# Kernel optimization log

Measured on AMD Instinct MI355X. Metric: run time of the kernel, lower is better.

Reference implementation:

```python
import jax, jax.numpy as jnp
import numpy as np
import math

D_HEAD = 64  # scaling uses sqrt(d_head), NOT sqrt of full projection dim (faithful to source)

def setup_inputs() -> dict:
    key = jax.random.key(0)
    ks = jax.random.split(key, 9)
    B, S, D = 4, 2048, 1024
    s = 0.02
    return {
        "x": jax.random.normal(ks[0], (B, S, D), dtype=jnp.float32),
        "Wq": jax.random.normal(ks[1], (D, D), dtype=jnp.float32) * s,
        "bq": jax.random.normal(ks[2], (D,), dtype=jnp.float32) * s,
        "Wk": jax.random.normal(ks[3], (D, D), dtype=jnp.float32) * s,
        "bk": jax.random.normal(ks[4], (D,), dtype=jnp.float32) * s,
        "Wv": jax.random.normal(ks[5], (D, D), dtype=jnp.float32) * s,
        "bv": jax.random.normal(ks[6], (D,), dtype=jnp.float32) * s,
        "Wo": jax.random.normal(ks[7], (D, D), dtype=jnp.float32) * s,
        "bo": jax.random.normal(ks[8], (D,), dtype=jnp.float32) * s,
    }

def reference(x, Wq, bq, Wk, bk, Wv, bv, Wo, bo):
    # Q/K/V projections: [B,S,D] @ [D,D] + b
    Q = jnp.einsum('bsd,de->bse', x, Wq) + bq
    K = jnp.einsum('bsd,de->bse', x, Wk) + bk
    V = jnp.einsum('bsd,de->bse', x, Wv) + bv
    # NOTE: source does bmm over the FULL projected dim (no head split),
    # scaled by sqrt(d_head) only.
    scores = jnp.einsum('bqd,bkd->bqk', Q, K) / math.sqrt(D_HEAD)  # [B,S,S]
    S_len = scores.shape[-1]
    causal = jnp.tril(jnp.ones((S_len, S_len), dtype=bool))
    scores = jnp.where(causal, scores, -jnp.inf)
    weights = jax.nn.softmax(scores, axis=-1)
    attn_out = jnp.einsum('bqk,bkd->bqd', weights, V)
    return jnp.einsum('bsd,de->bse', attn_out, Wo) + bo
```

## Files before the change

kernel.cpp:

```cpp
#include <hip/hip_runtime.h>
#include <stdint.h>

typedef _Float16 f16;
typedef __attribute__((ext_vector_type(8))) _Float16 f16x8;
typedef __attribute__((ext_vector_type(4))) _Float16 f16x4;
typedef __attribute__((ext_vector_type(4))) float f32x4;

typedef __attribute__((address_space(3))) uint32_t lds_u32;
typedef const __attribute__((address_space(1))) uint32_t glb_u32;

__device__ __forceinline__ void gload_lds16(const void* g, void* l) {
    __builtin_amdgcn_global_load_lds((glb_u32*)g, (lds_u32*)l, 16, 0, 0);
}


template<int ROWS>
__device__ __forceinline__
void stage2(const f16* __restrict__ G, int ldg, f16* lds,
            int grow0, int k0, int tid)
{
    const int l = tid & 63, w = tid >> 6;
    #pragma unroll
    for (int q = 0; q < ROWS / 32; ++q) {
        const int r = q * 32 + w * 8 + (l >> 3);
        const int csw = (((l & 7) ^ (r & 7)) << 3);
        gload_lds16(G + (long long)(grow0 + r) * ldg + (k0 + csw),
                    lds + q * 2048 + w * 512);
    }
}

template<int OUT_MODE, int CAUSAL, int TM, int TN>
__device__ __forceinline__
void gemm2_body(const f16* __restrict__ A, const f16* __restrict__ B,
                const float* __restrict__ bias, void* __restrict__ Cv,
                int M, int N, int K,
                long long sAb, long long sBb, long long sCb, float scale,
                int bx, int by, int bzi)
{
    constexpr int IM = TM / 32;
    constexpr int JN = TN / 32;

    int mtile, n0;
    if (CAUSAL == 1) {
        int rem = bx, mi = 0;
        while (rem > mi) { rem -= mi + 1; ++mi; }
        mtile = mi;
        n0 = rem * TN;
    } else {
        mtile = by;
        n0 = bx * TN;
    }

    const int tid  = threadIdx.x;
    const int wave = tid >> 6;
    const int lane = tid & 63;
    const long long bz = bzi;
    A += bz * sAb;
    B += bz * sBb;

    __shared__ f16 As[2][TM * 64];
    __shared__ f16 Bs[2][TN * 64];

    const int fr  = lane & 15;
    const int hk  = lane >> 4;
    const int lsw = lane & 7;
    const int wm  = (wave >> 1) * (TM / 2);
    const int wn  = (wave & 1) * (TN / 2);

    const int npass = (CAUSAL == 2) ? 2 : 1;
    for (int pass = 0; pass < npass; ++pass) {
        const int mt = (CAUSAL == 2 && pass == 1) ? (M / TM - 1 - mtile) : mtile;
        const int m0 = mt * TM;
        const int Kend = (CAUSAL == 2) ? (m0 + TM) : K;

        f32x4 acc[IM][JN] = {};

        stage2<TM>(A, K, &As[0][0], m0, 0, tid);
        stage2<TN>(B, K, &Bs[0][0], n0, 0, tid);
        asm volatile("s_waitcnt vmcnt(0)" ::: "memory");
        __builtin_amdgcn_s_barrier();

        int cur = 0;
        for (int k0 = 0; k0 < Kend; k0 += 64) {
            if (k0 + 64 < Kend) {
                stage2<TM>(A, K, &As[cur ^ 1][0], m0, k0 + 64, tid);
                stage2<TN>(B, K, &Bs[cur ^ 1][0], n0, k0 + 64, tid);
            }

            f16x8 af[IM][2], bf[JN][2];
            #pragma unroll
            for (int i = 0; i < IM; ++i)
                #pragma unroll
                for (int kk = 0; kk < 2; ++kk)
                    af[i][kk] = *(const f16x8*)((const char*)&As[cur][0] +
                        ((wm + i * 16 + fr) << 7) +
                        ((((kk << 2) | hk) ^ lsw) << 4));
            #pragma unroll
            for (int j = 0; j < JN; ++j)
                #pragma unroll
                for (int kk = 0; kk < 2; ++kk)
                    bf[j][kk] = *(const f16x8*)((const char*)&Bs[cur][0] +
                        ((wn + j * 16 + fr) << 7) +
                        ((((kk << 2) | hk) ^ lsw) << 4));

            asm volatile("s_waitcnt lgkmcnt(0)" ::: "memory");
            __builtin_amdgcn_s_setprio(1);
            #pragma unroll
            for (int i = 0; i < IM; ++i)
                #pragma unroll
                for (int j = 0; j < JN; ++j)
                    #pragma unroll
                    for (int kk = 0; kk < 2; ++kk)
                        acc[i][j] = __builtin_amdgcn_mfma_f32_16x16x32_f16(
                            af[i][kk], bf[j][kk], acc[i][j], 0, 0, 0);
            __builtin_amdgcn_s_setprio(0);

            asm volatile("s_waitcnt vmcnt(0)" ::: "memory");
            __builtin_amdgcn_s_barrier();
            cur ^= 1;
        }

        const int cn = lane & 15;
        const int cm = (lane >> 4) * 4;
        #pragma unroll
        for (int j = 0; j < JN; ++j) {
            const int gn = n0 + wn + j * 16 + cn;
            #pragma unroll
            for (int i = 0; i < IM; ++i) {
                const int gm = m0 + wm + i * 16 + cm;
                if (OUT_MODE == 0) {
                    const float bv = bias ? bias[gn] : 0.f;
                    float* C = (float*)Cv + bz * sCb;
                    #pragma unroll
                    for (int r = 0; r < 4; ++r)
                        C[(long long)(gm + r) * N + gn] = acc[i][j][r] * scale + bv;
                } else {
                    const float bv = bias ? bias[(long long)bz * N + gn] : 0.f;
                    f16* C = (f16*)Cv + bz * sCb;
                    #pragma unroll
                    for (int r = 0; r < 4; ++r)
                        C[(long long)(gm + r) * N + gn] = (f16)(acc[i][j][r] * scale + bv);
                }
            }
        }
    }
}

template<int OUT_MODE, int CAUSAL, int TM, int TN>
__global__ __launch_bounds__(256, 2)
void gemm2_bt(const f16* __restrict__ A, const f16* __restrict__ B,
              const float* __restrict__ bias, void* __restrict__ Cv,
              int M, int N, int K,
              long long sAb, long long sBb, long long sCb, float scale)
{
    gemm2_body<OUT_MODE, CAUSAL, TM, TN>(A, B, bias, Cv, M, N, K,
                                         sAb, sBb, sCb, scale,
                                         blockIdx.x, blockIdx.y, blockIdx.z);
}


__device__ __forceinline__
void stage_half(const f16* __restrict__ G, int ldg, f16* lds_half,
                int grow0, int k0, int tid)
{
    const int lr  = tid >> 3;
    const int csw = ((tid & 7) * 8) ^ ((lr & 7) << 3);
    gload_lds16(G + (long long)(grow0 + lr) * ldg + (k0 + csw),
                lds_half + ((tid >> 6) << 9));
    gload_lds16(G + (long long)(grow0 + 64 + lr) * ldg + (k0 + csw),
                lds_half + 4096 + ((tid >> 6) << 9));
}

template<int MODE>
__global__ __launch_bounds__(512, 2)
void gemm256_4ph(const f16* __restrict__ A, const f16* __restrict__ B,
                 const float* __restrict__ bias, const float* __restrict__ bias2,
                 f16* __restrict__ C0, f16* __restrict__ C1,
                 int M, int N, int K,
                 long long sAb, long long sBb, long long sCb, float scale)
{
    __shared__ f16 lds[65536];

    const int nwg  = gridDim.x;
    const int orig = blockIdx.x;
    const int swz  = (orig & 7) * (nwg >> 3) + (orig >> 3);

    int m0, n0;
    long long bz = 0;
    if (MODE == 1) {
        const int nr  = M >> 8;
        const int per = nr * (nr + 1) / 2;
        bz = swz / per;
        int rem = swz - (int)bz * per, mi = 0;
        while (rem > mi) { rem -= mi + 1; ++mi; }
        m0 = mi << 8;
        n0 = rem << 8;
    } else {
        const int ntn = N >> 8;
        const int mt = swz / ntn, nt = swz - mt * ntn;
        m0 = mt << 8;
        n0 = nt << 8;
    }
    A += bz * sAb;
    B += bz * sBb;

    const int tid  = threadIdx.x;
    const int lane = tid & 63;
    const int wave = tid >> 6;
    const int wm = (wave >> 2) << 7;
    const int wn = (wave & 3) << 6;
    const int fr  = lane & 15;
    const int hk  = lane >> 4;
    const int lsw = lane & 7;
    const int nkt = K >> 6;

    f32x4 acc[8][4] = {};
    f16x8 bf[4][2];

    stage_half(A, K, lds,         m0,       0, tid);
    stage_half(A, K, lds + 8192,  m0 + 128, 0, tid);
    stage_half(B, K, lds + 32768, n0,       0, tid);
    stage_half(B, K, lds + 40960, n0 + 128, 0, tid);
    if (nkt > 1) {
        stage_half(B, K, lds + 49152, n0,       64, tid);
        stage_half(B, K, lds + 57344, n0 + 128, 64, tid);
        asm volatile("s_waitcnt vmcnt(4)" ::: "memory");
    } else {
        asm volatile("s_waitcnt vmcnt(0)" ::: "memory");
    }
    __builtin_amdgcn_s_barrier();

    for (int t = 0; t < nkt; ++t) {
        const f16* Ab = lds + (t & 1) * 16384;
        const f16* Bb = lds + 32768 + (t & 1) * 16384;
        #pragma unroll
        for (int p = 0; p < 4; ++p) {
            if (p == 0) {
                #pragma unroll
                for (int j = 0; j < 4; ++j)
                    #pragma unroll
                    for (int kk = 0; kk < 2; ++kk)
                        bf[j][kk] = *(const f16x8*)((const char*)Bb +
                            ((wn + j * 16 + fr) << 7) +
                            ((((kk << 2) | hk) ^ lsw) << 4));
            }
            f16x8 af[2][2];
            #pragma unroll
            for (int ii = 0; ii < 2; ++ii)
                #pragma unroll
                for (int kk = 0; kk < 2; ++kk)
                    af[ii][kk] = *(const f16x8*)((const char*)Ab +
                        ((wm + (2 * p + ii) * 16 + fr) << 7) +
                        ((((kk << 2) | hk) ^ lsw) << 4));

            if (p == 0 && t + 1 < nkt)
                stage_half(A, K, lds + ((t + 1) & 1) * 16384,        m0,       (t + 1) << 6, tid);
            if (p == 1 && t + 1 < nkt)
                stage_half(A, K, lds + ((t + 1) & 1) * 16384 + 8192, m0 + 128, (t + 1) << 6, tid);
            if (p == 2 && t + 2 < nkt)
                stage_half(B, K, lds + 32768 + (t & 1) * 16384,        n0,       (t + 2) << 6, tid);
            if (p == 3 && t + 2 < nkt)
                stage_half(B, K, lds + 32768 + (t & 1) * 16384 + 8192, n0 + 128, (t + 2) << 6, tid);

            if (p == 0) asm volatile("s_waitcnt lgkmcnt(8)" ::: "memory");
            __builtin_amdgcn_s_barrier();
            asm volatile("s_waitcnt lgkmcnt(0)" ::: "memory");
            __builtin_amdgcn_s_setprio(1);
            #pragma unroll
            for (int ii = 0; ii < 2; ++ii)
                #pragma unroll
                for (int j = 0; j < 4; ++j)
                    #pragma unroll
                    for (int kk = 0; kk < 2; ++kk)
                        acc[2 * p + ii][j] = __builtin_amdgcn_mfma_f32_16x16x32_f16(
                            af[ii][kk], bf[j][kk], acc[2 * p + ii][j], 0, 0, 0);
            __builtin_amdgcn_s_setprio(0);
            if (p == 3) {
                if (t + 2 < nkt) asm volatile("s_waitcnt vmcnt(4)" ::: "memory");
                else             asm volatile("s_waitcnt vmcnt(0)" ::: "memory");
            }
            __builtin_amdgcn_s_barrier();
        }
    }

    const int cn  = lane & 15;
    const int cm4 = (lane >> 4) * 4;

    if (MODE == 3 && (n0 >> 10)) {
        const int nn0 = n0 & 1023;
        const int b   = m0 >> 11, s0v = m0 & 2047;
        #pragma unroll
        for (int j = 0; j < 4; ++j) {
            const int nn_l = wn + j * 16 + cn;
            const float bb = bias2[nn0 + nn_l];
            const int X = (nn_l & 7) << 4;
            #pragma unroll
            for (int i = 0; i < 8; ++i) {
                const int s_l = wm + i * 16 + cm4;
                f16x4 pk;
                #pragma unroll
                for (int r = 0; r < 4; ++r)
                    pk[r] = (f16)(acc[i][j][r] + bb);
                *(f16x4*)((char*)lds + nn_l * 512 + ((s_l * 2) ^ X)) = pk;
            }
        }
        __syncthreads();
        #pragma unroll 4
        for (int rr = 0; rr < 32; ++rr) {
            const int nn_l = rr * 8 + wave;
            const int X = (nn_l & 7) << 4;
            const f16x4 v = *(const f16x4*)((const char*)lds + nn_l * 512 + ((lane * 8) ^ X));
            *(f16x4*)&C1[(long long)b * 2097152 + (long long)(nn0 + nn_l) * 2048 + s0v + lane * 4] = v;
        }
        return;
    }

    #pragma unroll
    for (int j = 0; j < 4; ++j) {
        const int gn = n0 + wn + j * 16 + cn;
        if (MODE == 3) {
            const int nn = gn & 1023;
            #pragma unroll
            for (int i = 0; i < 8; ++i) {
                const int gm = m0 + wm + i * 16 + cm4;
                #pragma unroll
                for (int r = 0; r < 4; ++r)
                    C0[(long long)(gm + r) * 1024 + nn] = (f16)acc[i][j][r];
            }
        } else {
            const float cbv = bias ? bias[bz * N + gn] : 0.f;
            f16* Cc = C0 + bz * sCb;
            #pragma unroll
            for (int i = 0; i < 8; ++i) {
                const int gm = m0 + wm + i * 16 + cm4;
                #pragma unroll
                for (int r = 0; r < 4; ++r)
                    Cc[(long long)(gm + r) * N + gn] = (f16)(acc[i][j][r] * scale + cbv);
            }
        }
    }
}

__global__ __launch_bounds__(256)
void prep(const float* __restrict__ x,  const float* __restrict__ Wq,
          const float* __restrict__ bq, const float* __restrict__ Wk,
          const float* __restrict__ Wv, const float* __restrict__ bv,
          const float* __restrict__ Wo,
          f16* __restrict__ xb,  f16* __restrict__ Wqf, f16* __restrict__ Wkf,
          f16* __restrict__ Wvf, f16* __restrict__ Wot,
          float* __restrict__ bvo, float* __restrict__ wvec)
{
    __shared__ f16 tile[32][33];
    __shared__ float red[4][64];
    const int t = threadIdx.x;
    int id = blockIdx.x;

    if (id < 8192) {
        const int i = (id * 256 + t) * 4;
        const float4 v = *(const float4*)&x[i];
        f16x4 o; o[0]=(f16)v.x; o[1]=(f16)v.y; o[2]=(f16)v.z; o[3]=(f16)v.w;
        *(f16x4*)&xb[i] = o;
        return;
    }
    id -= 8192;
    if (id < 3072) {
        const float* src = (id < 1024) ? Wq : (id < 2048) ? Wk : Wv;
        f16* dst = (id < 1024) ? Wqf : (id < 2048) ? Wkf : Wvf;
        const int i = ((id & 1023) * 256 + t) * 4;
        const float4 v = *(const float4*)&src[i];
        f16x4 o; o[0]=(f16)v.x; o[1]=(f16)v.y; o[2]=(f16)v.z; o[3]=(f16)v.w;
        *(f16x4*)&dst[i] = o;
        return;
    }
    id -= 3072;
    if (id < 1024) {
        const int bx = (id & 31) * 32, by = (id >> 5) * 32;
        const int tx = t & 31, ty = t >> 5;
        #pragma unroll
        for (int i = 0; i < 32; i += 8)
            tile[ty + i][tx] = (f16)Wo[(long long)(by + ty + i) * 1024 + (bx + tx)];
        __syncthreads();
        #pragma unroll
        for (int i = 0; i < 32; i += 8)
            Wot[(long long)(bx + ty + i) * 1024 + (by + tx)] = tile[tx][ty + i];
        return;
    }
    id -= 1024;
    if (id < 16) {
        const int e0 = id * 64;
        const int wave = t >> 6, lane = t & 63;
        float a0 = 0.f, a1 = 0.f, a2 = 0.f, a3 = 0.f;
        for (int i = 0; i < 256; i += 4) {
            const int k = wave * 256 + i;
            a0 += bv[k]     * Wo[(long long)k * 1024 + e0 + lane];
            a1 += bv[k + 1] * Wo[(long long)(k + 1) * 1024 + e0 + lane];
            a2 += bv[k + 2] * Wo[(long long)(k + 2) * 1024 + e0 + lane];
            a3 += bv[k + 3] * Wo[(long long)(k + 3) * 1024 + e0 + lane];
        }
        red[wave][lane] = (a0 + a1) + (a2 + a3);
        __syncthreads();
        if (wave == 0)
            bvo[e0 + lane] = red[0][lane] + red[1][lane] + red[2][lane] + red[3][lane];
        return;
    }
    id -= 16;
    {
        const int row = id * 4 + (t >> 6);
        const int lane = t & 63;
        const float* src = Wk + (long long)row * 1024;
        float a = 0.f;
        #pragma unroll
        for (int tt = 0; tt < 16; ++tt) a += src[lane + 64 * tt] * bq[lane + 64 * tt];
        #pragma unroll
        for (int o = 32; o > 0; o >>= 1) a += __shfl_down(a, o);
        if (lane == 0) wvec[row] = a * 0.125f;
    }
}

__global__ __launch_bounds__(256, 2)
void dual_weights_cvec(const f16* __restrict__ Wkf, const f16* __restrict__ Wqf,
                       const f16* __restrict__ Wot, const f16* __restrict__ Wvf,
                       f16* __restrict__ Wcat2,
                       const f16* __restrict__ xb, const float* __restrict__ wvec,
                       float* __restrict__ cbias)
{
    if (blockIdx.z == 2) {
        const int flat = blockIdx.y * 8 + blockIdx.x;
        const int wave = threadIdx.x >> 6, lane = threadIdx.x & 63;
        #pragma unroll 4
        for (int rr = 0; rr < 32; ++rr) {
            const int row = (flat * 4 + wave) * 32 + rr;
            const f16* src = xb + (long long)row * 1024;
            float a = 0.f;
            #pragma unroll
            for (int tt = 0; tt < 16; ++tt)
                a += (float)src[lane + 64 * tt] * wvec[lane + 64 * tt];
            #pragma unroll
            for (int o = 32; o > 0; o >>= 1) a += __shfl_down(a, o);
            if (lane == 0) cbias[row] = a;
        }
        return;
    }
    const f16* Ax = (blockIdx.z == 0) ? Wkf : Wot;
    const f16* Bx = (blockIdx.z == 0) ? Wqf : Wvf;
    f16* Cx = Wcat2 + (long long)blockIdx.z * 1024 * 1024;
    gemm2_body<1, 0, 128, 128>(Ax, Bx, nullptr, Cx,
                               1024, 1024, 1024, 0, 0, 0, 1.f,
                               blockIdx.x, blockIdx.y, 0);
}

__global__ __launch_bounds__(256)
void softmax_causal(const f16* __restrict__ Sc, f16* __restrict__ P, int S)
{
    const long long row = blockIdx.x;
    const int q = (int)(row % S);
    const f16* src = Sc + row * S;
    f16* dst = P + row * S;
    const int t = threadIdx.x;
    __shared__ float redm[4], reds[4];

    f16x8 vv = {};
    if (t * 8 <= q) vv = *(const f16x8*)&src[t * 8];
    float v[8];
    float mx = -3.0e38f;
    #pragma unroll
    for (int i = 0; i < 8; ++i) {
        const int k = t * 8 + i;
        v[i] = (float)vv[i];
        if (k <= q) mx = fmaxf(mx, v[i]);
    }
    #pragma unroll
    for (int o = 32; o > 0; o >>= 1) mx = fmaxf(mx, __shfl_down(mx, o));
    if ((t & 63) == 0) redm[t >> 6] = mx;
    __syncthreads();
    mx = fmaxf(fmaxf(redm[0], redm[1]), fmaxf(redm[2], redm[3]));

    float sum = 0.f;
    #pragma unroll
    for (int i = 0; i < 8; ++i) {
        const int k = t * 8 + i;
        v[i] = (k <= q) ? __expf(v[i] - mx) : 0.f;
        sum += v[i];
    }
    #pragma unroll
    for (int o = 32; o > 0; o >>= 1) sum += __shfl_down(sum, o);
    if ((t & 63) == 0) reds[t >> 6] = sum;
    __syncthreads();
    sum = reds[0] + reds[1] + reds[2] + reds[3];
    const float inv = 1.f / sum;
    const int kend = ((q >> 7) + 1) << 7;
    if (t * 8 < kend) {
        f16x8 ov;
        #pragma unroll
        for (int i = 0; i < 8; ++i) ov[i] = (f16)(v[i] * inv);
        *(f16x8*)&dst[t * 8] = ov;
    }
}

extern "C" void kernel_launch(void* const* d_in, const int* in_sizes, int n_in,
                              void* d_out, int out_size, void* d_ws, size_t ws_size,
                              hipStream_t stream)
{
    const float* x  = (const float*)d_in[0];
    const float* Wq = (const float*)d_in[1];
    const float* bq = (const float*)d_in[2];
    const float* Wk = (const float*)d_in[3];
    const float* Wv = (const float*)d_in[5];
    const float* bv = (const float*)d_in[6];
    const float* Wo = (const float*)d_in[7];
    const float* bo = (const float*)d_in[8];
    float* out = (float*)d_out;

    const int B = 4, S = 2048, D = 1024;
    const long long SD  = (long long)S * D;
    const long long SS  = (long long)S * S;
    const long long BSD = (long long)B * SD;
    const int MS = B * S;

    char* p = (char*)d_ws;
    f16*   xb    = (f16*)p;  p += BSD * 2;
    f16*   Wqf   = (f16*)p;  p += (long long)D * D * 2;
    f16*   Wkf   = (f16*)p;  p += (long long)D * D * 2;
    f16*   Wvf   = (f16*)p;  p += (long long)D * D * 2;
    f16*   Wot   = (f16*)p;  p += (long long)D * D * 2;
    f16*   Wcat2 = (f16*)p;  p += 2LL * D * D * 2;
    float* bvo   = (float*)p; p += D * 4;
    float* wvec  = (float*)p; p += D * 4;
    float* cbias = (float*)p; p += (long long)MS * 4;
    f16*   Qh    = (f16*)p;  p += BSD * 2;
    f16*   Vt    = (f16*)p;  p += BSD * 2;
    f16*   Sc    = (f16*)p;  p += (long long)B * SS * 2;
    f16*   Pb    = (f16*)p;  p += (long long)B * SS * 2;

    dim3 blk(256);

    prep<<<dim3(12560), blk, 0, stream>>>(x, Wq, bq, Wk, Wv, bv, Wo,
                                          xb, Wqf, Wkf, Wvf, Wot, bvo, wvec);

    dual_weights_cvec<<<dim3(8, 8, 3), blk, 0, stream>>>(Wkf, Wqf, Wot, Wvf,
                                                         Wcat2, xb, wvec, cbias);

    dim3 gproj((MS / 256) * (2 * D / 256));
    gemm256_4ph<3><<<gproj, dim3(512), 0, stream>>>(xb, Wcat2, nullptr, bvo,
                                                    Qh, Vt,
                                                    MS, 2 * D, D, 0, 0, 0, 1.f);

    dim3 gsc(144);
    gemm256_4ph<1><<<gsc, dim3(512), 0, stream>>>(Qh, xb, cbias, nullptr,
                                                  Sc, nullptr,
                                                  S, S, D, SD, SD, SS, 0.125f);

    softmax_causal<<<dim3((unsigned)(B * S)), blk, 0, stream>>>(Sc, Pb, S);

    dim3 gpv(D / 64, S / 128 / 2, B);
    gemm2_bt<0, 2, 128, 64><<<gpv, blk, 0, stream>>>(Pb, Vt, bo, out,
                                                     S, D, S, SS, SD, SD, 1.f);
}
```

Before: 245.0 us.

## Triple-buffer LDS staging in GEMM with partial vmcnt waits

Extends the GEMM main loop from double to triple buffering in LDS, prefetching two K-tiles ahead. Each iteration waits only for the older tile's loads by using a vmcnt equal to one tile's load count, instead of draining every outstanding global load. This is meant to hide more global-memory latency behind the MFMA work. In exchange it raises LDS use by half, which may reduce occupancy, and it depends on the vmcnt literal matching the number of loads issued per tile.

Result: slower. 249.9 us (+2.0%).

```diff
diff --git a/kernel.cpp b/kernel.cpp
--- a/kernel.cpp
+++ b/kernel.cpp
@@ -11,6 +11,13 @@
 
 __device__ __forceinline__ void gload_lds16(const void* g, void* l) {
     __builtin_amdgcn_global_load_lds((glb_u32*)g, (lds_u32*)l, 16, 0, 0);
+}
+
+template<int N> __device__ __forceinline__ void waitcnt_vm() {
+    static_assert(N == 0 || N == 6 || N == 8, "unsupported vmcnt literal");
+    if constexpr (N == 0) asm volatile("s_waitcnt vmcnt(0)" ::: "memory");
+    else if constexpr (N == 6) asm volatile("s_waitcnt vmcnt(6)" ::: "memory");
+    else if constexpr (N == 8) asm volatile("s_waitcnt vmcnt(8)" ::: "memory");
 }
 
 
@@ -39,6 +46,7 @@
 {
     constexpr int IM = TM / 32;
     constexpr int JN = TN / 32;
+    constexpr int LT = TM / 32 + TN / 32;
 
     int mtile, n0;
     if (CAUSAL == 1) {
@@ -58,8 +66,8 @@
     A += bz * sAb;
     B += bz * sBb;
 
-    __shared__ f16 As[2][TM * 64];
-    __shared__ f16 Bs[2][TN * 64];
+    __shared__ f16 As[3][TM * 64];
+    __shared__ f16 Bs[3][TN * 64];
 
     const int fr  = lane & 15;
     const int hk  = lane >> 4;
@@ -72,34 +80,45 @@
         const int mt = (CAUSAL == 2 && pass == 1) ? (M / TM - 1 - mtile) : mtile;
         const int m0 = mt * TM;
         const int Kend = (CAUSAL == 2) ? (m0 + TM) : K;
+        const int nt = Kend >> 6;
 
         f32x4 acc[IM][JN] = {};
 
         stage2<TM>(A, K, &As[0][0], m0, 0, tid);
         stage2<TN>(B, K, &Bs[0][0], n0, 0, tid);
-        asm volatile("s_waitcnt vmcnt(0)" ::: "memory");
+        if (nt > 1) {
+            stage2<TM>(A, K, &As[1][0], m0, 64, tid);
+            stage2<TN>(B, K, &Bs[1][0], n0, 64, tid);
+            waitcnt_vm<LT>();
+        } else {
+            waitcnt_vm<0>();
+        }
         __builtin_amdgcn_s_barrier();
 
-        int cur = 0;
-        for (int k0 = 0; k0 < Kend; k0 += 64) {
-            if (k0 + 64 < Kend) {
-                stage2<TM>(A, K, &As[cur ^ 1][0], m0, k0 + 64, tid);
-                stage2<TN>(B, K, &Bs[cur ^ 1][0], n0, k0 + 64, tid);
-            }
-
+        for (int t = 0; t < nt; ++t) {
+            const int k0 = t << 6;
+            if (t + 2 < nt) {
+                f16* bufA = &As[(t + 2) % 3][0];
+                f16* bufB = &Bs[(t + 2) % 3][0];
+                stage2<TM>(A, K, bufA, m0, k0 + 128, tid);
+                stage2<TN>(B, K, bufB, n0, k0 + 128, tid);
+            }
+
+            const f16* Ab = &As[t % 3][0];
+            const f16* Bb = &Bs[t % 3][0];
             f16x8 af[IM][2], bf[JN][2];
             #pragma unroll
             for (int i = 0; i < IM; ++i)
                 #pragma unroll
                 for (int kk = 0; kk < 2; ++kk)
-                    af[i][kk] = *(const f16x8*)((const char*)&As[cur][0] +
+                    af[i][kk] = *(const f16x8*)((const char*)Ab +
                         ((wm + i * 16 + fr) << 7) +
                         ((((kk << 2) | hk) ^ lsw) << 4));
             #pragma unroll
             for (int j = 0; j < JN; ++j)
                 #pragma unroll
                 for (int kk = 0; kk < 2; ++kk)
-                    bf[j][kk] = *(const f16x8*)((const char*)&Bs[cur][0] +
+                    bf[j][kk] = *(const f16x8*)((const char*)Bb +
                         ((wn + j * 16 + fr) << 7) +
                         ((((kk << 2) | hk) ^ lsw) << 4));
 
@@ -115,9 +134,9 @@
                             af[i][kk], bf[j][kk], acc[i][j], 0, 0, 0);
             __builtin_amdgcn_s_setprio(0);
 
-            asm volatile("s_waitcnt vmcnt(0)" ::: "memory");
+            if (t + 2 < nt) waitcnt_vm<LT>();
+            else            waitcnt_vm<0>();
             __builtin_amdgcn_s_barrier();
-            cur ^= 1;
         }
 
         const int cn = lane & 15;
```
